# Performance work log

Hardware: AMD Instinct MI355X
Metric: run time of the kernel (lower is better)

Reference implementation:

```python
import jax, jax.numpy as jnp
import numpy as np
import math

NATOM = 20000
NEIGH = 600000
NWAVE = 8
MAX_L = 3
CUTOFF = 5.0
EMB_NL = [16, 16]
J_SEQ = [[1, 1, 0], [1, 1, 2], [2, 2, 2], [2, 2, 0], [1, 2, 3], [3, 3, 2]]
NSPH = (MAX_L + 1) ** 2


def wigner_3j(j1, j2, j3, m1, m2, m3):
    """Exact Wigner 3j symbol via the Racah formula (python ints -> float)."""
    f = math.factorial
    if m1 + m2 + m3 != 0:
        return 0.0
    pre = math.sqrt(
        f(j1 + j2 - j3) * f(j1 - j2 + j3) * f(-j1 + j2 + j3) / f(j1 + j2 + j3 + 1)
        * f(j1 + m1) * f(j1 - m1) * f(j2 + m2) * f(j2 - m2) * f(j3 + m3) * f(j3 - m3))
    tmin = max(0, j2 - j3 - m1, j1 - j3 + m2)
    tmax = min(j1 + j2 - j3, j1 - m1, j2 + m2)
    s = 0.0
    for t in range(tmin, tmax + 1):
        s += (-1) ** t / (f(t) * f(j3 - j2 + m1 + t) * f(j3 - j1 - m2 + t)
                          * f(j1 + j2 - j3 - t) * f(j1 - m1 - t) * f(j2 + m2 - t))
    return ((-1) ** (j1 - j2 - m3)) * pre * s


def real_sph(u, max_l):
    """Real spherical harmonics Y_{l,m}(u) for unit vectors u of shape (3, N).
    Output shape ((max_l+1)^2, N), flat index k = l*(l+1) + m, m in [-l, l]."""
    x, y, z = u[0], u[1], u[2]
    phi = jnp.arctan2(y, x)
    s = jnp.sqrt(jnp.clip(1.0 - z * z, 0.0))  # sin(theta)
    P = {(0, 0): jnp.ones_like(z)}
    for m in range(1, max_l + 1):
        P[(m, m)] = -(2 * m - 1) * s * P[(m - 1, m - 1)]
    for m in range(0, max_l):
        P[(m + 1, m)] = (2 * m + 1) * z * P[(m, m)]
    for m in range(0, max_l + 1):
        for l in range(m + 2, max_l + 1):
            P[(l, m)] = ((2 * l - 1) * z * P[(l - 1, m)] - (l + m - 1) * P[(l - 2, m)]) / (l - m)
    out = []
    for l in range(max_l + 1):
        for m in range(-l, l + 1):
            am = abs(m)
            K = math.sqrt((2 * l + 1) / (4.0 * math.pi) * math.factorial(l - am) / math.factorial(l + am))
            if m == 0:
                out.append(K * P[(l, 0)])
            elif m > 0:
                out.append(math.sqrt(2.0) * K * jnp.cos(m * phi) * P[(l, m)])
            else:
                out.append(math.sqrt(2.0) * K * jnp.sin(am * phi) * P[(l, am)])
    return jnp.stack(out)


def setup_inputs() -> dict:
    key = jax.random.key(0)
    ks = jax.random.split(key, 8)
    cart = jax.random.normal(ks[0], (3, NATOM), jnp.float32) * 10.0
    atomindex = jax.random.randint(ks[1], (2, NEIGH), 0, NATOM)
    shifts = jax.random.normal(ks[2], (3, NEIGH), jnp.float32)  # keeps distances > 0
    species = jax.random.uniform(ks[3], (NATOM,), jnp.float32)
    W1 = jax.random.normal(ks[4], (1, EMB_NL[0]), jnp.float32)
    b1 = jnp.zeros((EMB_NL[0],), jnp.float32)
    W2 = jax.random.normal(ks[5], (EMB_NL[0], EMB_NL[1]), jnp.float32) / math.sqrt(EMB_NL[0])
    b2 = jnp.zeros((EMB_NL[1],), jnp.float32)
    W3 = jax.random.normal(ks[6], (EMB_NL[1], 3 * NWAVE), jnp.float32) / math.sqrt(EMB_NL[1])
    b3 = jnp.zeros((3 * NWAVE,), jnp.float32)
    return {"cart": cart, "atomindex": atomindex, "shifts": shifts, "species": species,
            "W1": W1, "b1": b1, "W2": W2, "b2": b2, "W3": W3, "b3": b3}


def reference(cart, atomindex, shifts, species, W1, b1, W2, b2, W3, b3):
    natom = cart.shape[1]
    # edge vectors and distances
    coor = cart[:, atomindex[1]] - cart[:, atomindex[0]] + shifts  # (3, Neigh)
    dist = jnp.linalg.norm(coor, axis=0)                            # (Neigh,)
    # per-atom embedding MLP -> radial coefficients / gaussian params
    h = jax.nn.silu(species[:, None] @ W1 + b1)
    h = jax.nn.silu(h @ W2 + b2)
    emb = h @ W3 + b3                                               # (Natom, 3*nwave)
    expand = emb[atomindex[1]]                                      # (Neigh, 3*nwave)
    coeff = expand[:, :NWAVE]
    alpha = expand[:, NWAVE:2 * NWAVE]
    center = expand[:, 2 * NWAVE:]
    sd = alpha * (dist[:, None] - center)
    radial = jnp.exp(-sd * sd)                                      # (Neigh, nwave)
    cut = ((jnp.cos(dist / CUTOFF * jnp.pi) + 1.0) * 0.5) ** 3      # (Neigh,)
    sph = real_sph(coor / dist, MAX_L)                              # (NSPH, Neigh)
    equi = jnp.einsum('i,ij,ij,ki->ikj', cut, radial, coeff, sph)   # (Neigh, NSPH, nwave)
    sum_sph = jnp.zeros((natom, NSPH, NWAVE), sph.dtype).at[atomindex[0]].add(equi)
    sum_sph = sum_sph.transpose(1, 0, 2)                            # (NSPH, Natom, nwave)
    dens = []
    for J in J_SEQ:
        num = [j * (j + 1) for j in J]
        acc = jnp.zeros((natom, NWAVE), sph.dtype)
        for m1 in range(-J[0], J[0] + 1):
            for m2 in range(max(-J[2] - m1, -J[1]), min(J[2] - m1, J[1]) + 1):
                m3 = -m1 - m2
                w = wigner_3j(J[0], J[1], J[2], m1, m2, m3)
                acc = acc + sum_sph[num[0] + m1] * sum_sph[num[1] + m2] * sum_sph[num[2] + m3] * w
        dens.append(acc)
    return jnp.stack(dens)  # (nseq, Natom, nwave)
```

## Files before the change

kernel.cpp:

```cpp
#include <hip/hip_runtime.h>
#include <math.h>
#include <algorithm>
#include <string.h>

#define NATOM 20000
#define NEIGH 600000
#define NWAVE 8
#define NSPH 16
#define CAP 96

struct CFT {
  float v[6][7][7];
};

__device__ __forceinline__ float silu_f(float x) { return x / (1.f + expf(-x)); }

__global__ __launch_bounds__(256) void zero_kernel(int* __restrict__ counts)
{
  int t = blockIdx.x * 256 + threadIdx.x;
  if (t < NATOM) counts[t] = 0;
}

__global__ __launch_bounds__(256) void emb_scatter_kernel(
    const float* __restrict__ species, const float* __restrict__ cart,
    const float* __restrict__ W1, const float* __restrict__ b1,
    const float* __restrict__ W2, const float* __restrict__ b2,
    const float* __restrict__ W3, const float* __restrict__ b3,
    float4* __restrict__ emb4, float4* __restrict__ cart4,
    const int* __restrict__ aidx, const float* __restrict__ shifts,
    int* __restrict__ counts, float4* __restrict__ sortrec)
{
  int t = blockIdx.x * 256 + threadIdx.x;
  if (t < NATOM) {
    float spv = species[t];
    float h1[16], h2[16], e24[24];
#pragma unroll
    for (int c = 0; c < 16; ++c) {
      float v = spv * W1[c] + b1[c];
      h1[c] = silu_f(v);
    }
#pragma unroll
    for (int d = 0; d < 16; ++d) {
      float v = b2[d];
#pragma unroll
      for (int c = 0; c < 16; ++c) v += h1[c] * W2[c * 16 + d];
      h2[d] = silu_f(v);
    }
#pragma unroll
    for (int e = 0; e < 24; ++e) {
      float v = b3[e];
#pragma unroll
      for (int c = 0; c < 16; ++c) v += h2[c] * W3[c * 24 + e];
      e24[e] = v;
    }
    float4* dst = emb4 + (size_t)t * 8;
#pragma unroll
    for (int w = 0; w < 8; ++w)
      dst[w] = make_float4(e24[w], e24[8 + w], e24[16 + w], 0.f);
    cart4[t] = make_float4(cart[t], cart[NATOM + t], cart[2 * NATOM + t], 0.f);
  }
  if (t < NEIGH) {
    int i = aidx[t];
    int rank = atomicAdd(&counts[i], 1);
    float4 r;
    r.x = __int_as_float(aidx[NEIGH + t]);
    r.y = shifts[t];
    r.z = shifts[NEIGH + t];
    r.w = shifts[2 * NEIGH + t];
    sortrec[(size_t)i * CAP + rank] = r;
  }
}

__global__ __launch_bounds__(256) void fused_kernel(
    const float4* __restrict__ cart4, const float4* __restrict__ sortrec,
    const float4* __restrict__ emb4, const int* __restrict__ counts,
    float* __restrict__ out, CFT cf)
{
  int t = blockIdx.x * 256 + threadIdx.x;
  int a = t >> 5;
  int sub = t & 31;
  int wp = sub & 3;
  int q = sub >> 2;

  float4 ci = cart4[a];
  int s0 = a * CAP;
  int s1 = s0 + counts[a];

  float acc0[NSPH], acc1[NSPH];
#pragma unroll
  for (int k = 0; k < NSPH; ++k) { acc0[k] = 0.f; acc1[k] = 0.f; }

  const float SQ2 = 1.41421356237309515f;
  for (int s = s0 + q; s < s1; s += 8) {
    float4 r = sortrec[s];
    int j = __float_as_int(r.x);
    float4 cj = cart4[j];
    float cx = cj.x - ci.x + r.y;
    float cy = cj.y - ci.y + r.z;
    float cz = cj.z - ci.z + r.w;
    float d2 = cx * cx + cy * cy + cz * cz;
    float inv = __frsqrt_rn(d2);
    float dist = d2 * inv;
    float x = cx * inv, y = cy * inv, z = cz * inv;

    float cc = __cosf(dist * 0.62831853071795864769f);
    float cut0 = (cc + 1.f) * 0.5f;
    float cut = cut0 * cut0 * cut0;

    float4 e0 = emb4[(size_t)j * 8 + wp];
    float4 e1 = emb4[(size_t)j * 8 + wp + 4];
    float sd0 = e0.y * (dist - e0.z);
    float av0 = cut * e0.x * __expf(-sd0 * sd0);
    float sd1 = e1.y * (dist - e1.z);
    float av1 = cut * e1.x * __expf(-sd1 * sd1);

    float r2 = x * x + y * y;
    float ri = __frsqrt_rn(fmaxf(r2, 1e-30f));
    float cp = x * ri, sp = y * ri;
    float c2 = cp * cp - sp * sp, s2 = 2.f * cp * sp;
    float c3 = c2 * cp - s2 * sp, s3 = s2 * cp + c2 * sp;

    float sz = sqrtf(fmaxf(1.f - z * z, 0.f));
    float P11 = -sz;
    float P22 = -3.f * sz * P11;
    float P33 = -5.f * sz * P22;
    float P10 = z;
    float P21 = 3.f * z * P11;
    float P32 = 5.f * z * P22;
    float P20 = (3.f * z * P10 - 1.f) * 0.5f;
    float P31 = (5.f * z * P21 - 3.f * P11) * 0.5f;
    float P30 = (5.f * z * P20 - 2.f * P10) * (1.f / 3.f);

    float sph[NSPH];
    sph[0]  = 0.28209479177387814f;
    sph[1]  = SQ2 * 0.3454941494713355f  * sp * P11;
    sph[2]  = 0.4886025119029199f * P10;
    sph[3]  = SQ2 * 0.3454941494713355f  * cp * P11;
    sph[4]  = SQ2 * 0.12875806734106326f * s2 * P22;
    sph[5]  = SQ2 * 0.25751613468212653f * sp * P21;
    sph[6]  = 0.6307831305050401f * P20;
    sph[7]  = SQ2 * 0.25751613468212653f * cp * P21;
    sph[8]  = SQ2 * 0.12875806734106326f * c2 * P22;
    sph[9]  = SQ2 * 0.027814921575518937f * s3 * P33;
    sph[10] = SQ2 * 0.06813236509555433f  * s2 * P32;
    sph[11] = SQ2 * 0.2154534560761003f   * sp * P31;
    sph[12] = 0.7463526651802308f * P30;
    sph[13] = SQ2 * 0.2154534560761003f   * cp * P31;
    sph[14] = SQ2 * 0.06813236509555433f  * c2 * P32;
    sph[15] = SQ2 * 0.027814921575518937f * c3 * P33;

#pragma unroll
    for (int k = 0; k < NSPH; ++k) {
      acc0[k] += sph[k] * av0;
      acc1[k] += sph[k] * av1;
    }
  }

#pragma unroll
  for (int k = 0; k < NSPH; ++k) {
    acc0[k] += __shfl_xor(acc0[k], 4);
    acc0[k] += __shfl_xor(acc0[k], 8);
    acc0[k] += __shfl_xor(acc0[k], 16);
    acc1[k] += __shfl_xor(acc1[k], 4);
    acc1[k] += __shfl_xor(acc1[k], 8);
    acc1[k] += __shfl_xor(acc1[k], 16);
  }

  constexpr int J0s[6] = {1, 1, 2, 2, 1, 3};
  constexpr int J1s[6] = {1, 1, 2, 2, 2, 3};
  constexpr int J2s[6] = {0, 2, 2, 0, 3, 2};
#pragma unroll
  for (int jj = 0; jj < 6; ++jj) {
    const int J0 = J0s[jj], J1 = J1s[jj], J2 = J2s[jj];
    const int n0 = J0 * (J0 + 1), n1 = J1 * (J1 + 1), n2 = J2 * (J2 + 1);
    float dj0 = 0.f, dj1 = 0.f;
#pragma unroll
    for (int m1 = -3; m1 <= 3; ++m1) {
      if (m1 < -J0 || m1 > J0) continue;
#pragma unroll
      for (int m2 = -3; m2 <= 3; ++m2) {
        if (m2 < -J1 || m2 > J1) continue;
        const int m3 = -m1 - m2;
        if (m3 < -J2 || m3 > J2) continue;
        const float w3 = cf.v[jj][m1 + 3][m2 + 3];
        dj0 += acc0[n0 + m1] * acc0[n1 + m2] * acc0[n2 + m3] * w3;
        dj1 += acc1[n0 + m1] * acc1[n1 + m2] * acc1[n2 + m3] * w3;
      }
    }
    if (q == jj) {
      out[((size_t)jj * NATOM + a) * 8 + wp]     = dj0;
      out[((size_t)jj * NATOM + a) * 8 + wp + 4] = dj1;
    }
  }
}

static double dfact(int n) { double r = 1.0; for (int i = 2; i <= n; ++i) r *= i; return r; }
static double wig3j(int j1, int j2, int j3, int m1, int m2, int m3) {
  if (m1 + m2 + m3 != 0) return 0.0;
  double pre = sqrt(dfact(j1 + j2 - j3) * dfact(j1 - j2 + j3) * dfact(-j1 + j2 + j3)
                    / dfact(j1 + j2 + j3 + 1)
                    * dfact(j1 + m1) * dfact(j1 - m1) * dfact(j2 + m2) * dfact(j2 - m2)
                    * dfact(j3 + m3) * dfact(j3 - m3));
  int tmin = std::max(0, std::max(j2 - j3 - m1, j1 - j3 + m2));
  int tmax = std::min(j1 + j2 - j3, std::min(j1 - m1, j2 + m2));
  double s = 0.0;
  for (int t = tmin; t <= tmax; ++t)
    s += ((t & 1) ? -1.0 : 1.0) /
         (dfact(t) * dfact(j3 - j2 + m1 + t) * dfact(j3 - j1 - m2 + t) *
          dfact(j1 + j2 - j3 - t) * dfact(j1 - m1 - t) * dfact(j2 + m2 - t));
  int e = j1 - j2 - m3;
  double sgn = ((e % 2) != 0) ? -1.0 : 1.0;
  return sgn * pre * s;
}

extern "C" void kernel_launch(void* const* d_in, const int* in_sizes, int n_in,
                              void* d_out, int out_size, void* d_ws, size_t ws_size,
                              hipStream_t stream)
{
  const float* cart    = (const float*)d_in[0];
  const int*   aidx    = (const int*)d_in[1];
  const float* shifts  = (const float*)d_in[2];
  const float* species = (const float*)d_in[3];
  const float* W1 = (const float*)d_in[4];
  const float* b1 = (const float*)d_in[5];
  const float* W2 = (const float*)d_in[6];
  const float* b2 = (const float*)d_in[7];
  const float* W3 = (const float*)d_in[8];
  const float* b3 = (const float*)d_in[9];
  float* out = (float*)d_out;

  float4* sortrec = (float4*)d_ws;
  float4* emb4    = sortrec + (size_t)NATOM * CAP;
  float4* cart4   = emb4 + (size_t)NATOM * 8;
  int*    counts  = (int*)(cart4 + NATOM);

  static const int JS[6][3] = {{1,1,0},{1,1,2},{2,2,2},{2,2,0},{1,2,3},{3,3,2}};
  CFT cf;
  memset(&cf, 0, sizeof(cf));
  for (int j = 0; j < 6; ++j) {
    int J0 = JS[j][0], J1 = JS[j][1], J2 = JS[j][2];
    for (int m1 = -J0; m1 <= J0; ++m1)
      for (int m2 = std::max(-J2 - m1, -J1); m2 <= std::min(J2 - m1, J1); ++m2) {
        int m3 = -m1 - m2;
        cf.v[j][m1 + 3][m2 + 3] = (float)wig3j(J0, J1, J2, m1, m2, m3);
      }
  }

  zero_kernel<<<(NATOM + 255) / 256, 256, 0, stream>>>(counts);
  emb_scatter_kernel<<<(NEIGH + 255) / 256, 256, 0, stream>>>(
      species, cart, W1, b1, W2, b2, W3, b3, emb4, cart4, aidx, shifts, counts, sortrec);
  fused_kernel<<<(NATOM * 32) / 256, 256, 0, stream>>>(
      cart4, sortrec, emb4, counts, out, cf);
}
```

Before: 77.90 us.

## Use one wavefront per atom with one wave per lane and prefetch neighbor loads

The fused kernel now assigns a full 64-lane wavefront to each atom, with each lane handling one radial wave instead of two, so twice as many threads run with half the accumulator registers each. The neighbor loop is software-pipelined to prefetch the next neighbor's record, coordinates and embedding while the current one is computed. In the scatter kernel the atomicAdd is moved after the record loads. The spherical-harmonic math is now recomputed by 8 lanes per neighbor instead of 4, which doubles that redundant work in exchange for more parallelism and latency hiding.

After: 85.81 us. 10.2% more time.

```diff
diff --git a/kernel.cpp b/kernel.cpp
--- a/kernel.cpp
+++ b/kernel.cpp
@@ -61,12 +61,12 @@
   }
   if (t < NEIGH) {
     int i = aidx[t];
-    int rank = atomicAdd(&counts[i], 1);
     float4 r;
     r.x = __int_as_float(aidx[NEIGH + t]);
     r.y = shifts[t];
     r.z = shifts[NEIGH + t];
     r.w = shifts[2 * NEIGH + t];
+    int rank = atomicAdd(&counts[i], 1);
     sortrec[(size_t)i * CAP + rank] = r;
   }
 }
@@ -77,24 +77,44 @@
     float* __restrict__ out, CFT cf)
 {
   int t = blockIdx.x * 256 + threadIdx.x;
-  int a = t >> 5;
-  int sub = t & 31;
-  int wp = sub & 3;
-  int q = sub >> 2;
+  int a = t >> 6;
+  int lane = t & 63;
+  int w = lane & 7;
+  int q = lane >> 3;
 
   float4 ci = cart4[a];
   int s0 = a * CAP;
   int s1 = s0 + counts[a];
 
-  float acc0[NSPH], acc1[NSPH];
-#pragma unroll
-  for (int k = 0; k < NSPH; ++k) { acc0[k] = 0.f; acc1[k] = 0.f; }
+  float acc[NSPH];
+#pragma unroll
+  for (int k = 0; k < NSPH; ++k) acc[k] = 0.f;
 
   const float SQ2 = 1.41421356237309515f;
-  for (int s = s0 + q; s < s1; s += 8) {
-    float4 r = sortrec[s];
+
+  int s = s0 + q;
+  bool valid = s < s1;
+  float4 r  = make_float4(0.f, 0.f, 0.f, 0.f);
+  float4 cj = r, e0 = r;
+  if (valid) {
+    r = sortrec[s];
     int j = __float_as_int(r.x);
-    float4 cj = cart4[j];
+    cj = cart4[j];
+    e0 = emb4[(size_t)j * 8 + w];
+  }
+
+  while (valid) {
+    int sn = s + 8;
+    bool vn = sn < s1;
+    float4 rn  = make_float4(0.f, 0.f, 0.f, 0.f);
+    float4 cjn = rn, e0n = rn;
+    if (vn) {
+      rn = sortrec[sn];
+      int jn = __float_as_int(rn.x);
+      cjn = cart4[jn];
+      e0n = emb4[(size_t)jn * 8 + w];
+    }
+
     float cx = cj.x - ci.x + r.y;
     float cy = cj.y - ci.y + r.z;
     float cz = cj.z - ci.z + r.w;
@@ -107,12 +127,8 @@
     float cut0 = (cc + 1.f) * 0.5f;
     float cut = cut0 * cut0 * cut0;
 
-    float4 e0 = emb4[(size_t)j * 8 + wp];
-    float4 e1 = emb4[(size_t)j * 8 + wp + 4];
     float sd0 = e0.y * (dist - e0.z);
-    float av0 = cut * e0.x * __expf(-sd0 * sd0);
-    float sd1 = e1.y * (dist - e1.z);
-    float av1 = cut * e1.x * __expf(-sd1 * sd1);
+    float av = cut * e0.x * __expf(-sd0 * sd0);
 
     float r2 = x * x + y * y;
     float ri = __frsqrt_rn(fmaxf(r2, 1e-30f));
@@ -150,20 +166,16 @@
     sph[15] = SQ2 * 0.027814921575518937f * c3 * P33;
 
 #pragma unroll
-    for (int k = 0; k < NSPH; ++k) {
-      acc0[k] += sph[k] * av0;
-      acc1[k] += sph[k] * av1;
-    }
+    for (int k = 0; k < NSPH; ++k) acc[k] += sph[k] * av;
+
+    s = sn; valid = vn; r = rn; cj = cjn; e0 = e0n;
   }
 
 #pragma unroll
   for (int k = 0; k < NSPH; ++k) {
-    acc0[k] += __shfl_xor(acc0[k], 4);
-    acc0[k] += __shfl_xor(acc0[k], 8);
-    acc0[k] += __shfl_xor(acc0[k], 16);
-    acc1[k] += __shfl_xor(acc1[k], 4);
-    acc1[k] += __shfl_xor(acc1[k], 8);
-    acc1[k] += __shfl_xor(acc1[k], 16);
+    acc[k] += __shfl_xor(acc[k], 8);
+    acc[k] += __shfl_xor(acc[k], 16);
+    acc[k] += __shfl_xor(acc[k], 32);
   }
 
   constexpr int J0s[6] = {1, 1, 2, 2, 1, 3};
@@ -173,7 +185,7 @@
   for (int jj = 0; jj < 6; ++jj) {
     const int J0 = J0s[jj], J1 = J1s[jj], J2 = J2s[jj];
     const int n0 = J0 * (J0 + 1), n1 = J1 * (J1 + 1), n2 = J2 * (J2 + 1);
-    float dj0 = 0.f, dj1 = 0.f;
+    float dj = 0.f;
 #pragma unroll
     for (int m1 = -3; m1 <= 3; ++m1) {
       if (m1 < -J0 || m1 > J0) continue;
@@ -182,15 +194,11 @@
         if (m2 < -J1 || m2 > J1) continue;
         const int m3 = -m1 - m2;
         if (m3 < -J2 || m3 > J2) continue;
-        const float w3 = cf.v[jj][m1 + 3][m2 + 3];
-        dj0 += acc0[n0 + m1] * acc0[n1 + m2] * acc0[n2 + m3] * w3;
-        dj1 += acc1[n0 + m1] * acc1[n1 + m2] * acc1[n2 + m3] * w3;
+        dj += acc[n0 + m1] * acc[n1 + m2] * acc[n2 + m3] * cf.v[jj][m1 + 3][m2 + 3];
       }
     }
-    if (q == jj) {
-      out[((size_t)jj * NATOM + a) * 8 + wp]     = dj0;
-      out[((size_t)jj * NATOM + a) * 8 + wp + 4] = dj1;
-    }
+    if (q == jj)
+      out[((size_t)jj * NATOM + a) * 8 + w] = dj;
   }
 }
 
@@ -249,6 +257,6 @@
   zero_kernel<<<(NATOM + 255) / 256, 256, 0, stream>>>(counts);
   emb_scatter_kernel<<<(NEIGH + 255) / 256, 256, 0, stream>>>(
       species, cart, W1, b1, W2, b2, W3, b3, emb4, cart4, aidx, shifts, counts, sortrec);
-  fused_kernel<<<(NATOM * 32) / 256, 256, 0, stream>>>(
+  fused_kernel<<<(NATOM * 64) / 256, 256, 0, stream>>>(
       cart4, sortrec, emb4, counts, out, cf);
 }
```
